# Performance work log

Measured on AMD Instinct MI355X. Metric: run time of the kernel, lower is better.

The kernel has to match this reference:

```python
import jax, jax.numpy as jnp
import numpy as np

D_EMBED = 1024
N_HEADS = 16
D_HEAD = 64
D_MLP = 4096
SEQ = 2048
BATCH = 2
ALPHA = 1.0


def setup_inputs() -> dict:
    key = jax.random.key(0)
    ks = jax.random.split(key, 7)
    s = ALPHA / np.sqrt(D_EMBED)
    return {
        "x": jax.random.normal(ks[0], (BATCH, SEQ, D_EMBED), jnp.float32),
        "W_K": s * jax.random.normal(ks[1], (N_HEADS, D_HEAD, D_EMBED), jnp.float32),
        "W_Q": s * jax.random.normal(ks[2], (N_HEADS, D_HEAD, D_EMBED), jnp.float32),
        "W_V": s * jax.random.normal(ks[3], (N_HEADS, D_HEAD, D_EMBED), jnp.float32),
        "W_O": s * jax.random.normal(ks[4], (D_EMBED, N_HEADS * D_HEAD), jnp.float32),
        "W_in": s * jax.random.normal(ks[5], (D_MLP, D_EMBED), jnp.float32),
        "b_in": jnp.zeros((D_MLP,), jnp.float32),
        "W_out": s * jax.random.normal(ks[6], (D_EMBED, D_MLP), jnp.float32),
        "b_out": jnp.zeros((D_EMBED,), jnp.float32),
    }


def reference(x, W_K, W_Q, W_V, W_O, W_in, b_in, W_out, b_out):
    b, c_len, _ = x.shape
    d_head = W_K.shape[1]
    # q/k/v: [batch, head, ctx, d_head]
    k = jnp.einsum('ahe,bce->bach', W_K, x)
    q = jnp.einsum('ahe,bce->bach', W_Q, x)
    v = jnp.einsum('ahe,bce->bach', W_V, x)
    # scores[b,a,c,C] = k_c . q_C  (faithful to original index convention)
    scores = jnp.einsum('bach,baCh->bacC', k, q)
    mask = jnp.tril(jnp.ones((c_len, c_len), dtype=x.dtype))  # [c, C]
    masked = scores * mask - 1e10 * (1.0 - mask)
    attn = jax.nn.softmax(masked / np.sqrt(d_head), axis=-1)  # softmax over C (query idx)
    # z[b,a,C,h] = sum_c v[b,a,c,h] * attn[b,a,c,C]
    z = jnp.einsum('bach,bacC->baCh', v, attn)
    z_flat = jnp.transpose(z, (0, 2, 1, 3)).reshape(b, c_len, -1)  # [b, c, a*h]
    attn_out = jnp.einsum('ef,bcf->bce', W_O, z_flat)
    x = x + attn_out
    h = jnp.einsum('me,bce->bcm', W_in, x) + b_in
    h = jax.nn.relu(h)
    mlp_out = jnp.einsum('em,bcm->bce', W_out, h) + b_out
    return x + mlp_out
```

## Files before the change

kernel.cpp:

```cpp
#include <hip/hip_runtime.h>
#include <hip/hip_bf16.h>
#include <cstdint>
#include <cstddef>

typedef __bf16 bf16;
typedef bf16 bf16x4 __attribute__((ext_vector_type(4)));
typedef bf16 bf16x8 __attribute__((ext_vector_type(8)));
typedef float floatx4 __attribute__((ext_vector_type(4)));
typedef float floatx16 __attribute__((ext_vector_type(16)));
typedef unsigned int uint;

#define MFMA16(a, b, c) __builtin_amdgcn_mfma_f32_16x16x32_bf16((a), (b), (c), 0, 0, 0)
#define MFMA32(a, b, c) __builtin_amdgcn_mfma_f32_32x32x16_bf16((a), (b), (c), 0, 0, 0)

#define K2 0.18033688011112042f

__device__ __forceinline__ void async16(const void* g, void* l) {
    __builtin_amdgcn_global_load_lds((const __attribute__((address_space(1))) void*)g,
                                     (__attribute__((address_space(3))) void*)l,
                                     16, 0, 0);
}

__device__ __forceinline__ void stage64s(const bf16* g0, int ldg, bf16* lds, int wave, int lane) {
#pragma unroll
    for (int i = 0; i < 2; ++i) {
        int r0 = wave * 16 + i * 8;
        async16(g0 + (size_t)(r0 + (lane >> 3)) * ldg + ((lane & 7) ^ (lane >> 3)) * 8,
                lds + r0 * 64);
    }
}
__device__ __forceinline__ bf16x8 rd64(const bf16* t, int row, int chunk) {
    return *(const bf16x8*)&t[row * 64 + ((chunk ^ (row & 7)) * 8)];
}
__device__ __forceinline__ bf16x8 rd32(const bf16* t, int row, int quad) {
    return *(const bf16x8*)&t[row * 32 + ((quad ^ (row & 3)) * 8)];
}

__device__ __forceinline__ uint pk2(float lo, float hi) {
    union { bf16 h[2]; uint u; } c;
    c.h[0] = (bf16)lo;
    c.h[1] = (bf16)hi;
    return c.u;
}

__global__ __launch_bounds__(256) void cvt_all(const float* __restrict__ x,
                                               const float* __restrict__ WQ,
                                               const float* __restrict__ WK,
                                               const float* __restrict__ WV,
                                               const float* __restrict__ WO,
                                               const float* __restrict__ Win,
                                               const float* __restrict__ Wout,
                                               bf16* __restrict__ xb,
                                               bf16* __restrict__ wqkv,
                                               bf16* __restrict__ wo,
                                               bf16* __restrict__ win,
                                               bf16* __restrict__ wout) {
    int blk = blockIdx.x;
    const float* src;
    bf16* dst;
    int off;
    if (blk < 1024)      { src = WQ;   dst = wqkv;           off = blk; }
    else if (blk < 2048) { src = WK;   dst = wqkv + 1048576; off = blk - 1024; }
    else if (blk < 3072) { src = WV;   dst = wqkv + 2097152; off = blk - 2048; }
    else if (blk < 4096) { src = WO;   dst = wo;             off = blk - 3072; }
    else if (blk < 8192) { src = Win;  dst = win;            off = blk - 4096; }
    else if (blk < 12288){ src = Wout; dst = wout;           off = blk - 8192; }
    else                 { src = x;    dst = xb;             off = blk - 12288; }
    int i = off * 1024 + threadIdx.x * 4;
    float4 v = *(const float4*)(src + i);
    bf16x4 o = {(bf16)v.x, (bf16)v.y, (bf16)v.z, (bf16)v.w};
    *(bf16x4*)(dst + i) = o;
}

template <int EPI, int NACC>
__device__ __forceinline__ void epilogue(floatx4 (&acc)[4][NACC], int m0, int n0,
                                         int wm, int wn, int col, int quad,
                                         float* Cf, bf16* Cb, int ldc,
                                         const float* bias, const float* res) {
#pragma unroll
    for (int mi = 0; mi < 4; ++mi)
#pragma unroll
        for (int ni = 0; ni < NACC; ++ni)
#pragma unroll
            for (int r = 0; r < 4; ++r) {
                int row = m0 + wm + mi * 16 + quad * 4 + r;
                int cc = n0 + wn + ni * 16 + col;
                size_t idx = (size_t)row * ldc + cc;
                float v = acc[mi][ni][r];
                if constexpr (EPI == 0) {
                    Cb[idx] = (bf16)v;
                } else if constexpr (EPI == 1) {
                    v += res[idx];
                    Cf[idx] = v;
                    Cb[idx] = (bf16)v;
                } else if constexpr (EPI == 2) {
                    v += bias[cc];
                    v = fmaxf(v, 0.f);
                    Cb[idx] = (bf16)v;
                } else {
                    v += bias[cc] + Cf[idx];
                    Cf[idx] = v;
                }
            }
}

template <int EPI>
__global__ __launch_bounds__(256) void gemm_pipe(const bf16* __restrict__ A, int lda,
                                                 const bf16* __restrict__ B, int ldb, int K,
                                                 float* __restrict__ Cf, bf16* __restrict__ Cb,
                                                 int ldc, const float* __restrict__ bias,
                                                 const float* __restrict__ res) {
    __shared__ __align__(16) bf16 As[3][128 * 32];
    __shared__ __align__(16) bf16 Bs[3][128 * 32];
    const int tid = threadIdx.x, wave = tid >> 6, lane = tid & 63;
    const int m0 = blockIdx.y * 128, n0 = blockIdx.x * 128;
    const int wm = (wave >> 1) * 64, wn = (wave & 1) * 64;
    const int col = lane & 15, quad = lane >> 4;
    const int cs8 = ((lane & 3) ^ ((lane >> 2) & 3)) * 8;

    floatx4 acc[4][4];
#pragma unroll
    for (int mi = 0; mi < 4; ++mi)
#pragma unroll
        for (int ni = 0; ni < 4; ++ni) acc[mi][ni] = (floatx4){0.f, 0.f, 0.f, 0.f};

    auto stage = [&](int buf, int k0) {
#pragma unroll
        for (int i = 0; i < 2; ++i) {
            int r0 = wave * 32 + i * 16;
            async16(A + (size_t)(m0 + r0 + (lane >> 2)) * lda + k0 + cs8,
                    As[buf] + r0 * 32);
            async16(B + (size_t)(n0 + r0 + (lane >> 2)) * ldb + k0 + cs8,
                    Bs[buf] + r0 * 32);
        }
    };

    const int nk = K / 32;
    stage(0, 0);
    stage(1, 32);
    for (int it = 0; it < nk; ++it) {
        if (it + 1 < nk) asm volatile("s_waitcnt vmcnt(4)" ::: "memory");
        else             asm volatile("s_waitcnt vmcnt(0)" ::: "memory");
        __builtin_amdgcn_s_barrier();
        if (it + 2 < nk) stage((it + 2) % 3, (it + 2) * 32);

        const bf16* as = As[it % 3];
        const bf16* bs = Bs[it % 3];
        bf16x8 af[4], bfr[4];
#pragma unroll
        for (int mi = 0; mi < 4; ++mi) af[mi] = rd32(as, wm + mi * 16 + col, quad);
#pragma unroll
        for (int ni = 0; ni < 4; ++ni) bfr[ni] = rd32(bs, wn + ni * 16 + col, quad);
#pragma unroll
        for (int mi = 0; mi < 4; ++mi)
#pragma unroll
            for (int ni = 0; ni < 4; ++ni)
                acc[mi][ni] = MFMA16(af[mi], bfr[ni], acc[mi][ni]);
    }
    epilogue<EPI, 4>(acc, m0, n0, wm, wn, col, quad, Cf, Cb, ldc, bias, res);
}

template <int EPI>
__global__ __launch_bounds__(256) void gemm97s(const bf16* __restrict__ A, int lda,
                                               const bf16* __restrict__ B, int ldb, int K,
                                               float* __restrict__ Cf, bf16* __restrict__ Cb,
                                               int ldc, const float* __restrict__ bias,
                                               const float* __restrict__ res) {
    __shared__ __align__(16) bf16 As[128 * 64];
    __shared__ __align__(16) bf16 Bs[64 * 64];
    const int tid = threadIdx.x, wave = tid >> 6, lane = tid & 63;
    const int m0 = blockIdx.y * 128, n0 = blockIdx.x * 64;
    const int wm = (wave >> 1) * 64, wn = (wave & 1) * 32;
    const int col = lane & 15, quad = lane >> 4;

    floatx4 acc[4][2];
#pragma unroll
    for (int mi = 0; mi < 4; ++mi)
#pragma unroll
        for (int ni = 0; ni < 2; ++ni) acc[mi][ni] = (floatx4){0.f, 0.f, 0.f, 0.f};

    const int rsub = lane >> 3;
    const int csub = ((lane & 7) ^ rsub) * 8;

    for (int k0 = 0; k0 < K; k0 += 64) {
        __syncthreads();
#pragma unroll
        for (int i = 0; i < 4; ++i) {
            int r0 = wave * 32 + i * 8;
            async16(A + (size_t)(m0 + r0 + rsub) * lda + k0 + csub, As + r0 * 64);
        }
#pragma unroll
        for (int i = 0; i < 2; ++i) {
            int r0 = wave * 16 + i * 8;
            async16(B + (size_t)(n0 + r0 + rsub) * ldb + k0 + csub, Bs + r0 * 64);
        }
        __syncthreads();

#pragma unroll
        for (int ks = 0; ks < 2; ++ks) {
            bf16x8 af[4], bfr[2];
#pragma unroll
            for (int mi = 0; mi < 4; ++mi) {
                int row = wm + mi * 16 + col;
                af[mi] = *(const bf16x8*)&As[row * 64 + (((ks * 4 + quad) ^ (row & 7)) * 8)];
            }
#pragma unroll
            for (int ni = 0; ni < 2; ++ni) {
                int row = wn + ni * 16 + col;
                bfr[ni] = *(const bf16x8*)&Bs[row * 64 + (((ks * 4 + quad) ^ (row & 7)) * 8)];
            }
#pragma unroll
            for (int mi = 0; mi < 4; ++mi)
#pragma unroll
                for (int ni = 0; ni < 2; ++ni)
                    acc[mi][ni] = MFMA16(af[mi], bfr[ni], acc[mi][ni]);
        }
    }
    epilogue<EPI, 2>(acc, m0, n0, wm, wn, col, quad, Cf, Cb, ldc, bias, res);
}

__global__ __launch_bounds__(256) void transpose_v(const bf16* __restrict__ qkv,
                                                   const float* __restrict__ linv,
                                                   bf16* __restrict__ vt) {
    __shared__ bf16 t[64][65];
    const int bh = blockIdx.y, ct = blockIdx.x;
    const int b = bh >> 4, a = bh & 15;
    const float* lv = linv + (size_t)bh * 2048 + ct * 64;
    for (int idx = threadIdx.x; idx < 4096; idx += 256) {
        int c = idx >> 6, h = idx & 63;
        float v = (float)qkv[(size_t)(b * 2048 + ct * 64 + c) * 3072 + 2048 + a * 64 + h];
        t[h][c] = (bf16)(v * lv[c]);
    }
    __syncthreads();
    for (int idx = threadIdx.x; idx < 4096; idx += 256) {
        int h = idx >> 6, c = idx & 63;
        vt[(size_t)(bh * 64 + h) * 2048 + ct * 64 + c] = t[h][c];
    }
}

__global__ __launch_bounds__(256) void attn_stats(const bf16* __restrict__ qkv,
                                                  float* __restrict__ linv) {
    __shared__ __align__(16) bf16 Kt[64 * 64];
    __shared__ __align__(16) bf16 Qt[3][64 * 64];
    const int xx = blockIdx.x;
    const int ct = (xx & 1) ? (31 - (xx >> 1)) : (xx >> 1);
    const int bh = blockIdx.y;
    const int b = bh >> 4, a = bh & 15;
    const int tid = threadIdx.x, wave = tid >> 6, lane = tid & 63;
    const int col = lane & 15, quad = lane >> 4;
    const bf16* base = qkv + (size_t)b * 2048 * 3072;

    stage64s(base + (size_t)ct * 64 * 3072 + 1024 + a * 64, 3072, Kt, wave, lane);
    stage64s(base + a * 64, 3072, Qt[0], wave, lane);
    if (ct >= 1) stage64s(base + (size_t)1 * 64 * 3072 + a * 64, 3072, Qt[1], wave, lane);

    float lrun[4] = {0.f, 0.f, 0.f, 0.f};
    bf16x8 a0, a1;

    for (int Ct = 0; Ct <= ct; ++Ct) {
        if (Ct < ct) asm volatile("s_waitcnt vmcnt(2)" ::: "memory");
        else         asm volatile("s_waitcnt vmcnt(0)" ::: "memory");
        __builtin_amdgcn_s_barrier();
        if (Ct + 2 <= ct)
            stage64s(base + (size_t)(Ct + 2) * 64 * 3072 + a * 64, 3072,
                     Qt[(Ct + 2) % 3], wave, lane);
        if (Ct == 0) {
            a0 = rd64(Kt, wave * 16 + col, quad);
            a1 = rd64(Kt, wave * 16 + col, quad + 4);
        }
        const bf16* q = Qt[Ct % 3];
#pragma unroll
        for (int nt = 0; nt < 4; ++nt) {
            bf16x8 b0 = rd64(q, nt * 16 + col, quad);
            bf16x8 b1 = rd64(q, nt * 16 + col, quad + 4);
            floatx4 sacc = (floatx4){0.f, 0.f, 0.f, 0.f};
            sacc = MFMA16(a0, b0, sacc);
            sacc = MFMA16(a1, b1, sacc);
#pragma unroll
            for (int r = 0; r < 4; ++r) {
                float e = __builtin_amdgcn_exp2f(sacc[r] * K2);
                if (Ct == ct && (nt * 16 + col) > (wave * 16 + quad * 4 + r)) e = 0.f;
                lrun[r] += e;
            }
        }
    }
#pragma unroll
    for (int r = 0; r < 4; ++r) {
        float t = lrun[r];
        t += __shfl_xor(t, 1);
        t += __shfl_xor(t, 2);
        t += __shfl_xor(t, 4);
        t += __shfl_xor(t, 8);
        lrun[r] = t;
    }
    if (col == 0) {
#pragma unroll
        for (int r = 0; r < 4; ++r) {
            int c = ct * 64 + wave * 16 + quad * 4 + r;
            linv[(size_t)bh * 2048 + c] = 1.0f / lrun[r];
        }
    }
}

__global__ __launch_bounds__(256) void attn_av(const bf16* __restrict__ qkv,
                                               const bf16* __restrict__ vt,
                                               bf16* __restrict__ zb) {
    __shared__ __align__(16) bf16 Qt[64 * 64];
    __shared__ __align__(16) bf16 Kt[3][64 * 64];
    __shared__ __align__(16) bf16 Vt[3][64 * 64];
    const int xx = blockIdx.x;
    const int Ctile = (xx & 1) ? (31 - (xx >> 1)) : (xx >> 1);
    const int bh = blockIdx.y;
    const int b = bh >> 4, a = bh & 15;
    const int tid = threadIdx.x, wave = tid >> 6, lane = tid & 63;
    const int l31 = lane & 31, lh = lane >> 5;
    const int cq = wave >> 1, Cq = wave & 1;
    const bf16* base = qkv + (size_t)b * 2048 * 3072;
    const int niter = 32 - Ctile;

    stage64s(base + (size_t)Ctile * 64 * 3072 + a * 64, 3072, Qt, wave, lane);
    stage64s(base + (size_t)Ctile * 64 * 3072 + 1024 + a * 64, 3072, Kt[0], wave, lane);
    stage64s(vt + (size_t)bh * 64 * 2048 + Ctile * 64, 2048, Vt[0], wave, lane);
    if (niter > 1) {
        stage64s(base + (size_t)(Ctile + 1) * 64 * 3072 + 1024 + a * 64, 3072, Kt[1], wave, lane);
        stage64s(vt + (size_t)bh * 64 * 2048 + (Ctile + 1) * 64, 2048, Vt[1], wave, lane);
    }

    floatx16 zacc[2];
    zacc[0] = (floatx16)0.f;
    zacc[1] = (floatx16)0.f;
    bf16x8 qf[4];

    for (int i = 0; i < niter; ++i) {
        const int ct = Ctile + i;
        if (i + 1 < niter) asm volatile("s_waitcnt vmcnt(4)" ::: "memory");
        else               asm volatile("s_waitcnt vmcnt(0)" ::: "memory");
        __builtin_amdgcn_s_barrier();
        if (i + 2 < niter) {
            stage64s(base + (size_t)(ct + 2) * 64 * 3072 + 1024 + a * 64, 3072,
                     Kt[(i + 2) % 3], wave, lane);
            stage64s(vt + (size_t)bh * 64 * 2048 + (ct + 2) * 64, 2048,
                     Vt[(i + 2) % 3], wave, lane);
        }
        if (i == 0) {
#pragma unroll
            for (int s = 0; s < 4; ++s) qf[s] = rd64(Qt, 32 * Cq + l31, 2 * s + lh);
        }
        const bf16* kt = Kt[i % 3];
        const bf16* vts = Vt[i % 3];

        floatx16 sacc = (floatx16)0.f;
        __builtin_amdgcn_s_setprio(1);
#pragma unroll
        for (int s = 0; s < 4; ++s) {
            bf16x8 kf = rd64(kt, 32 * cq + l31, 2 * s + lh);
            sacc = MFMA32(kf, qf[s], sacc);
        }
        __builtin_amdgcn_s_setprio(0);

        float p[16];
#pragma unroll
        for (int r = 0; r < 16; ++r) {
            float e = __builtin_amdgcn_exp2f(sacc[r] * K2);
            if (i == 0) {
                int creg = (r & 3) + 8 * (r >> 2) + 4 * lh;
                if (32 * Cq + l31 > 32 * cq + creg) e = 0.f;
            }
            p[r] = e;
        }

        bf16x8 pa[2];
#pragma unroll
        for (int g = 0; g < 2; ++g) {
            uint w0 = pk2(p[8 * g + 0], p[8 * g + 1]);
            uint w1 = pk2(p[8 * g + 2], p[8 * g + 3]);
            uint w2 = pk2(p[8 * g + 4], p[8 * g + 5]);
            uint w3 = pk2(p[8 * g + 6], p[8 * g + 7]);
            uint xw0 = (uint)__shfl_xor((int)w0, 32);
            uint xw1 = (uint)__shfl_xor((int)w1, 32);
            uint xw2 = (uint)__shfl_xor((int)w2, 32);
            uint xw3 = (uint)__shfl_xor((int)w3, 32);
            union { uint u[4]; bf16x8 v; } cv;
            cv.u[0] = lh ? xw2 : w0;
            cv.u[1] = lh ? xw3 : w1;
            cv.u[2] = lh ? w2 : xw0;
            cv.u[3] = lh ? w3 : xw1;
            pa[g] = cv.v;
        }

        __builtin_amdgcn_s_setprio(1);
#pragma unroll
        for (int ht = 0; ht < 2; ++ht) {
#pragma unroll
            for (int s = 0; s < 2; ++s) {
                bf16x8 vf = rd64(vts, 32 * ht + l31, 4 * cq + 2 * s + lh);
                zacc[ht] = MFMA32(pa[s], vf, zacc[ht]);
            }
        }
        __builtin_amdgcn_s_setprio(0);
    }

    __syncthreads();
    float* Zex = (float*)Kt;
    if (cq == 1) {
#pragma unroll
        for (int ht = 0; ht < 2; ++ht)
#pragma unroll
            for (int q = 0; q < 4; ++q) {
                float4 t4 = {zacc[ht][4 * q + 0], zacc[ht][4 * q + 1],
                             zacc[ht][4 * q + 2], zacc[ht][4 * q + 3]};
                *(float4*)&Zex[Cq * 2048 + lane * 32 + (((ht * 4 + q) ^ (lane & 7)) * 4)] = t4;
            }
    }
    __syncthreads();
    if (cq == 0) {
#pragma unroll
        for (int ht = 0; ht < 2; ++ht)
#pragma unroll
            for (int q = 0; q < 4; ++q) {
                float4 t4 = *(const float4*)&Zex[Cq * 2048 + lane * 32 +
                                                 (((ht * 4 + q) ^ (lane & 7)) * 4)];
                zacc[ht][4 * q + 0] += t4.x;
                zacc[ht][4 * q + 1] += t4.y;
                zacc[ht][4 * q + 2] += t4.z;
                zacc[ht][4 * q + 3] += t4.w;
            }
#pragma unroll
        for (int ht = 0; ht < 2; ++ht)
#pragma unroll
            for (int r = 0; r < 16; ++r) {
                int Cg = Ctile * 64 + 32 * Cq + (r & 3) + 8 * (r >> 2) + 4 * lh;
                zb[(size_t)(b * 2048 + Cg) * 1024 + a * 64 + 32 * ht + l31] =
                    (bf16)zacc[ht][r];
            }
    }
}

extern "C" void kernel_launch(void* const* d_in, const int* in_sizes, int n_in,
                              void* d_out, int out_size, void* d_ws, size_t ws_size,
                              hipStream_t stream) {
    (void)in_sizes; (void)n_in; (void)out_size; (void)ws_size;
    const float* x    = (const float*)d_in[0];
    const float* WK   = (const float*)d_in[1];
    const float* WQ   = (const float*)d_in[2];
    const float* WV   = (const float*)d_in[3];
    const float* WO   = (const float*)d_in[4];
    const float* Win  = (const float*)d_in[5];
    const float* bin  = (const float*)d_in[6];
    const float* Wout = (const float*)d_in[7];
    const float* bout = (const float*)d_in[8];
    float* out = (float*)d_out;

    char* ws = (char*)d_ws;
    bf16*  xb   = (bf16*)(ws + 0);
    bf16*  wqkv = (bf16*)(ws + 8388608);
    bf16*  wo   = (bf16*)(ws + 14680064);
    bf16*  win  = (bf16*)(ws + 16777216);
    bf16*  wout = (bf16*)(ws + 25165824);
    bf16*  qkvb = (bf16*)(ws + 33554432);
    bf16*  vtb  = (bf16*)(ws + 58720256);
    float* mst  = (float*)(ws + 67108864);
    bf16*  zbuf = (bf16*)(ws + 67633152);
    bf16*  xmid = (bf16*)(ws + 76021760);
    bf16*  hbuf = (bf16*)(ws + 84410368);

    cvt_all<<<16384, 256, 0, stream>>>(x, WQ, WK, WV, WO, Win, Wout,
                                       xb, wqkv, wo, win, wout);

    gemm_pipe<0><<<dim3(24, 32), 256, 0, stream>>>(xb, 1024, wqkv, 1024, 1024,
                                                   nullptr, qkvb, 3072, nullptr, nullptr);
    attn_stats<<<dim3(32, 32), 256, 0, stream>>>(qkvb, mst);
    transpose_v<<<dim3(32, 32), 256, 0, stream>>>(qkvb, mst, vtb);
    attn_av<<<dim3(32, 32), 256, 0, stream>>>(qkvb, vtb, zbuf);
    gemm97s<1><<<dim3(16, 32), 256, 0, stream>>>(zbuf, 1024, wo, 1024, 1024,
                                                 out, xmid, 1024, nullptr, x);
    gemm_pipe<2><<<dim3(32, 32), 256, 0, stream>>>(xmid, 1024, win, 1024, 1024,
                                                   nullptr, hbuf, 4096, bin, nullptr);
    gemm97s<3><<<dim3(16, 32), 256, 0, stream>>>(hbuf, 4096, wout, 4096, 4096,
                                                 out, nullptr, 1024, bout, nullptr);
}
```

Before: 398.1 us.

## Double attention tile size to 128 rows with 512-thread blocks

Result: faster. 381.4 us (-4.2%).

```diff
diff --git a/kernel.cpp b/kernel.cpp
--- a/kernel.cpp
+++ b/kernel.cpp
@@ -28,6 +28,11 @@
         async16(g0 + (size_t)(r0 + (lane >> 3)) * ldg + ((lane & 7) ^ (lane >> 3)) * 8,
                 lds + r0 * 64);
     }
+}
+__device__ __forceinline__ void stage64q(const bf16* g0, int ldg, bf16* lds, int wave, int lane) {
+    int r0 = wave * 8;
+    async16(g0 + (size_t)(r0 + (lane >> 3)) * ldg + ((lane & 7) ^ (lane >> 3)) * 8,
+            lds + r0 * 64);
 }
 __device__ __forceinline__ bf16x8 rd64(const bf16* t, int row, int chunk) {
     return *(const bf16x8*)&t[row * 64 + ((chunk ^ (row & 7)) * 8)];
@@ -238,93 +243,113 @@
     }
 }
 
-__global__ __launch_bounds__(256) void attn_stats(const bf16* __restrict__ qkv,
-                                                  float* __restrict__ linv) {
-    __shared__ __align__(16) bf16 Kt[64 * 64];
+__global__ __launch_bounds__(512, 4) void attn_stats(const bf16* __restrict__ qkv,
+                                                     float* __restrict__ linv) {
+    __shared__ __align__(16) bf16 Kt[128 * 64];
     __shared__ __align__(16) bf16 Qt[3][64 * 64];
+    __shared__ float red[4][32];
     const int xx = blockIdx.x;
-    const int ct = (xx & 1) ? (31 - (xx >> 1)) : (xx >> 1);
-    const int bh = blockIdx.y;
-    const int b = bh >> 4, a = bh & 15;
-    const int tid = threadIdx.x, wave = tid >> 6, lane = tid & 63;
-    const int col = lane & 15, quad = lane >> 4;
-    const bf16* base = qkv + (size_t)b * 2048 * 3072;
-
-    stage64s(base + (size_t)ct * 64 * 3072 + 1024 + a * 64, 3072, Kt, wave, lane);
-    stage64s(base + a * 64, 3072, Qt[0], wave, lane);
-    if (ct >= 1) stage64s(base + (size_t)1 * 64 * 3072 + a * 64, 3072, Qt[1], wave, lane);
-
-    float lrun[4] = {0.f, 0.f, 0.f, 0.f};
-    bf16x8 a0, a1;
-
-    for (int Ct = 0; Ct <= ct; ++Ct) {
-        if (Ct < ct) asm volatile("s_waitcnt vmcnt(2)" ::: "memory");
-        else         asm volatile("s_waitcnt vmcnt(0)" ::: "memory");
-        __builtin_amdgcn_s_barrier();
-        if (Ct + 2 <= ct)
-            stage64s(base + (size_t)(Ct + 2) * 64 * 3072 + a * 64, 3072,
-                     Qt[(Ct + 2) % 3], wave, lane);
-        if (Ct == 0) {
-            a0 = rd64(Kt, wave * 16 + col, quad);
-            a1 = rd64(Kt, wave * 16 + col, quad + 4);
-        }
-        const bf16* q = Qt[Ct % 3];
-#pragma unroll
-        for (int nt = 0; nt < 4; ++nt) {
-            bf16x8 b0 = rd64(q, nt * 16 + col, quad);
-            bf16x8 b1 = rd64(q, nt * 16 + col, quad + 4);
-            floatx4 sacc = (floatx4){0.f, 0.f, 0.f, 0.f};
-            sacc = MFMA16(a0, b0, sacc);
-            sacc = MFMA16(a1, b1, sacc);
-#pragma unroll
-            for (int r = 0; r < 4; ++r) {
-                float e = __builtin_amdgcn_exp2f(sacc[r] * K2);
-                if (Ct == ct && (nt * 16 + col) > (wave * 16 + quad * 4 + r)) e = 0.f;
-                lrun[r] += e;
-            }
-        }
-    }
-#pragma unroll
-    for (int r = 0; r < 4; ++r) {
-        float t = lrun[r];
-        t += __shfl_xor(t, 1);
-        t += __shfl_xor(t, 2);
-        t += __shfl_xor(t, 4);
-        t += __shfl_xor(t, 8);
-        lrun[r] = t;
-    }
-    if (col == 0) {
-#pragma unroll
-        for (int r = 0; r < 4; ++r) {
-            int c = ct * 64 + wave * 16 + quad * 4 + r;
-            linv[(size_t)bh * 2048 + c] = 1.0f / lrun[r];
-        }
-    }
-}
-
-__global__ __launch_bounds__(256) void attn_av(const bf16* __restrict__ qkv,
-                                               const bf16* __restrict__ vt,
-                                               bf16* __restrict__ zb) {
-    __shared__ __align__(16) bf16 Qt[64 * 64];
-    __shared__ __align__(16) bf16 Kt[3][64 * 64];
-    __shared__ __align__(16) bf16 Vt[3][64 * 64];
-    const int xx = blockIdx.x;
-    const int Ctile = (xx & 1) ? (31 - (xx >> 1)) : (xx >> 1);
+    const int t = (xx & 1) ? (15 - (xx >> 1)) : (xx >> 1);
     const int bh = blockIdx.y;
     const int b = bh >> 4, a = bh & 15;
     const int tid = threadIdx.x, wave = tid >> 6, lane = tid & 63;
     const int l31 = lane & 31, lh = lane >> 5;
-    const int cq = wave >> 1, Cq = wave & 1;
+    const int kq = wave & 3, qh = wave >> 2;
     const bf16* base = qkv + (size_t)b * 2048 * 3072;
-    const int niter = 32 - Ctile;
-
-    stage64s(base + (size_t)Ctile * 64 * 3072 + a * 64, 3072, Qt, wave, lane);
-    stage64s(base + (size_t)Ctile * 64 * 3072 + 1024 + a * 64, 3072, Kt[0], wave, lane);
-    stage64s(vt + (size_t)bh * 64 * 2048 + Ctile * 64, 2048, Vt[0], wave, lane);
-    if (niter > 1) {
-        stage64s(base + (size_t)(Ctile + 1) * 64 * 3072 + 1024 + a * 64, 3072, Kt[1], wave, lane);
-        stage64s(vt + (size_t)bh * 64 * 2048 + (Ctile + 1) * 64, 2048, Vt[1], wave, lane);
-    }
+    const int c0 = t * 128;
+    const int niter = 2 * t + 2;
+
+    stage64s(base + (size_t)c0 * 3072 + 1024 + a * 64, 3072, Kt, wave, lane);
+    stage64q(base + a * 64, 3072, Qt[0], wave, lane);
+    stage64q(base + (size_t)64 * 3072 + a * 64, 3072, Qt[1], wave, lane);
+
+    float lrun[16];
+#pragma unroll
+    for (int r = 0; r < 16; ++r) lrun[r] = 0.f;
+    bf16x8 kf[4];
+
+    for (int i = 0; i < niter; ++i) {
+        if (i + 1 < niter) asm volatile("s_waitcnt vmcnt(1)" ::: "memory");
+        else               asm volatile("s_waitcnt vmcnt(0)" ::: "memory");
+        __builtin_amdgcn_s_barrier();
+        if (i + 2 < niter)
+            stage64q(base + (size_t)(i + 2) * 64 * 3072 + a * 64, 3072,
+                     Qt[(i + 2) % 3], wave, lane);
+        if (i == 0) {
+#pragma unroll
+            for (int s = 0; s < 4; ++s) kf[s] = rd64(Kt, 32 * kq + l31, 2 * s + lh);
+        }
+        const bf16* q = Qt[i % 3];
+        bf16x8 qf0 = rd64(q, 32 * qh + l31, 0 + lh);
+        bf16x8 qf1 = rd64(q, 32 * qh + l31, 2 + lh);
+        bf16x8 qf2 = rd64(q, 32 * qh + l31, 4 + lh);
+        bf16x8 qf3 = rd64(q, 32 * qh + l31, 6 + lh);
+        floatx16 s0 = (floatx16)0.f, s1 = (floatx16)0.f;
+        __builtin_amdgcn_s_setprio(1);
+        s0 = MFMA32(kf[0], qf0, s0);
+        s1 = MFMA32(kf[2], qf2, s1);
+        s0 = MFMA32(kf[1], qf1, s0);
+        s1 = MFMA32(kf[3], qf3, s1);
+        __builtin_amdgcn_s_setprio(0);
+#pragma unroll
+        for (int r = 0; r < 16; ++r) {
+            float e = __builtin_amdgcn_exp2f((s0[r] + s1[r]) * K2);
+            if (i >= niter - 2) {
+                int Crel = 64 * (i - 2 * t) + 32 * qh + l31;
+                int crel = 32 * kq + (r & 3) + 8 * (r >> 2) + 4 * lh;
+                if (Crel > crel) e = 0.f;
+            }
+            lrun[r] += e;
+        }
+    }
+#pragma unroll
+    for (int r = 0; r < 16; ++r) {
+        float v = lrun[r];
+        v += __shfl_xor(v, 1);
+        v += __shfl_xor(v, 2);
+        v += __shfl_xor(v, 4);
+        v += __shfl_xor(v, 8);
+        v += __shfl_xor(v, 16);
+        lrun[r] = v;
+    }
+    if (qh == 1 && l31 == 0) {
+#pragma unroll
+        for (int r = 0; r < 16; ++r)
+            red[kq][(r & 3) + 8 * (r >> 2) + 4 * lh] = lrun[r];
+    }
+    __syncthreads();
+    if (qh == 0 && l31 == 0) {
+#pragma unroll
+        for (int r = 0; r < 16; ++r) {
+            int cr = (r & 3) + 8 * (r >> 2) + 4 * lh;
+            linv[(size_t)bh * 2048 + c0 + 32 * kq + cr] = 1.0f / (lrun[r] + red[kq][cr]);
+        }
+    }
+}
+
+__global__ __launch_bounds__(512, 4) void attn_av(const bf16* __restrict__ qkv,
+                                                  const bf16* __restrict__ vt,
+                                                  bf16* __restrict__ zb) {
+    __shared__ __align__(16) char smem[65536];
+    bf16* Qt = (bf16*)smem;
+    bf16* Kt = (bf16*)(smem + 16384);
+    bf16* Vt = (bf16*)(smem + 40960);
+    const int xx = blockIdx.x;
+    const int t = (xx & 1) ? (15 - (xx >> 1)) : (xx >> 1);
+    const int bh = blockIdx.y;
+    const int b = bh >> 4, a = bh & 15;
+    const int tid = threadIdx.x, wave = tid >> 6, lane = tid & 63;
+    const int l31 = lane & 31, lh = lane >> 5;
+    const int Cq = wave & 3, cq = wave >> 2;
+    const bf16* base = qkv + (size_t)b * 2048 * 3072;
+    const int C0 = t * 128;
+    const int niter = 32 - 2 * t;
+
+    stage64s(base + (size_t)C0 * 3072 + a * 64, 3072, Qt, wave, lane);
+    stage64q(base + (size_t)(2 * t) * 64 * 3072 + 1024 + a * 64, 3072, Kt, wave, lane);
+    stage64q(vt + (size_t)bh * 64 * 2048 + 2 * t * 64, 2048, Vt, wave, lane);
+    stage64q(base + (size_t)(2 * t + 1) * 64 * 3072 + 1024 + a * 64, 3072, Kt + 4096, wave, lane);
+    stage64q(vt + (size_t)bh * 64 * 2048 + (2 * t + 1) * 64, 2048, Vt + 4096, wave, lane);
 
     floatx16 zacc[2];
     zacc[0] = (floatx16)0.f;
@@ -332,39 +357,39 @@
     bf16x8 qf[4];
 
     for (int i = 0; i < niter; ++i) {
-        const int ct = Ctile + i;
-        if (i + 1 < niter) asm volatile("s_waitcnt vmcnt(4)" ::: "memory");
+        const int ct = 2 * t + i;
+        if (i + 1 < niter) asm volatile("s_waitcnt vmcnt(2)" ::: "memory");
         else               asm volatile("s_waitcnt vmcnt(0)" ::: "memory");
         __builtin_amdgcn_s_barrier();
         if (i + 2 < niter) {
-            stage64s(base + (size_t)(ct + 2) * 64 * 3072 + 1024 + a * 64, 3072,
-                     Kt[(i + 2) % 3], wave, lane);
-            stage64s(vt + (size_t)bh * 64 * 2048 + (ct + 2) * 64, 2048,
-                     Vt[(i + 2) % 3], wave, lane);
+            stage64q(base + (size_t)(ct + 2) * 64 * 3072 + 1024 + a * 64, 3072,
+                     Kt + ((i + 2) % 3) * 4096, wave, lane);
+            stage64q(vt + (size_t)bh * 64 * 2048 + (ct + 2) * 64, 2048,
+                     Vt + ((i + 2) % 3) * 4096, wave, lane);
         }
         if (i == 0) {
 #pragma unroll
             for (int s = 0; s < 4; ++s) qf[s] = rd64(Qt, 32 * Cq + l31, 2 * s + lh);
         }
-        const bf16* kt = Kt[i % 3];
-        const bf16* vts = Vt[i % 3];
-
-        floatx16 sacc = (floatx16)0.f;
+        const bf16* kt = Kt + (i % 3) * 4096;
+        const bf16* vts = Vt + (i % 3) * 4096;
+
+        floatx16 s0 = (floatx16)0.f, s1 = (floatx16)0.f;
         __builtin_amdgcn_s_setprio(1);
-#pragma unroll
-        for (int s = 0; s < 4; ++s) {
-            bf16x8 kf = rd64(kt, 32 * cq + l31, 2 * s + lh);
-            sacc = MFMA32(kf, qf[s], sacc);
-        }
+        s0 = MFMA32(rd64(kt, 32 * cq + l31, 0 + lh), qf[0], s0);
+        s1 = MFMA32(rd64(kt, 32 * cq + l31, 4 + lh), qf[2], s1);
+        s0 = MFMA32(rd64(kt, 32 * cq + l31, 2 + lh), qf[1], s0);
+        s1 = MFMA32(rd64(kt, 32 * cq + l31, 6 + lh), qf[3], s1);
         __builtin_amdgcn_s_setprio(0);
 
         float p[16];
 #pragma unroll
         for (int r = 0; r < 16; ++r) {
-            float e = __builtin_amdgcn_exp2f(sacc[r] * K2);
-            if (i == 0) {
-                int creg = (r & 3) + 8 * (r >> 2) + 4 * lh;
-                if (32 * Cq + l31 > 32 * cq + creg) e = 0.f;
+            float e = __builtin_amdgcn_exp2f((s0[r] + s1[r]) * K2);
+            if (i < 2) {
+                int Crel = 32 * Cq + l31;
+                int crel = 64 * i + 32 * cq + (r & 3) + 8 * (r >> 2) + 4 * lh;
+                if (Crel > crel) e = 0.f;
             }
             p[r] = e;
         }
@@ -401,7 +426,7 @@
     }
 
     __syncthreads();
-    float* Zex = (float*)Kt;
+    float* Zex = (float*)smem;
     if (cq == 1) {
 #pragma unroll
         for (int ht = 0; ht < 2; ++ht)
@@ -429,7 +454,7 @@
         for (int ht = 0; ht < 2; ++ht)
 #pragma unroll
             for (int r = 0; r < 16; ++r) {
-                int Cg = Ctile * 64 + 32 * Cq + (r & 3) + 8 * (r >> 2) + 4 * lh;
+                int Cg = C0 + 32 * Cq + (r & 3) + 8 * (r >> 2) + 4 * lh;
                 zb[(size_t)(b * 2048 + Cg) * 1024 + a * 64 + 32 * ht + l31] =
                     (bf16)zacc[ht][r];
             }
@@ -469,9 +494,9 @@
 
     gemm_pipe<0><<<dim3(24, 32), 256, 0, stream>>>(xb, 1024, wqkv, 1024, 1024,
                                                    nullptr, qkvb, 3072, nullptr, nullptr);
-    attn_stats<<<dim3(32, 32), 256, 0, stream>>>(qkvb, mst);
+    attn_stats<<<dim3(16, 32), 512, 0, stream>>>(qkvb, mst);
     transpose_v<<<dim3(32, 32), 256, 0, stream>>>(qkvb, mst, vtb);
-    attn_av<<<dim3(32, 32), 256, 0, stream>>>(qkvb, vtb, zbuf);
+    attn_av<<<dim3(16, 32), 512, 0, stream>>>(qkvb, vtb, zbuf);
     gemm97s<1><<<dim3(16, 32), 256, 0, stream>>>(zbuf, 1024, wo, 1024, 1024,
                                                  out, xmid, 1024, nullptr, x);
     gemm_pipe<2><<<dim3(32, 32), 256, 0, stream>>>(xmid, 1024, win, 1024, 1024,
```
